# Kernel tuning notes

Measured on AMD Instinct MI355X. Metric: run time of the kernel, lower is better.

## Reference

```python
import jax, jax.numpy as jnp
import numpy as np

B, S, D = 8, 1024, 1024
H, DK = 16, 64  # num_heads, d_k; H*DK == D
NEG_INF = 1e29


def setup_inputs() -> dict:
    key = jax.random.key(0)
    ks = jax.random.split(key, 12)
    sc = 1.0 / np.sqrt(D)
    q = jax.random.normal(ks[0], (B, S, D), jnp.float32)
    k = jax.random.normal(ks[1], (B, S, D), jnp.float32)
    v = jax.random.normal(ks[2], (B, S, D), jnp.float32)
    # causal mask, broadcast per batch (mask==0 positions are masked out)
    mask = jnp.broadcast_to(jnp.tril(jnp.ones((S, S), jnp.int32)), (B, S, S))
    Wq = jax.random.normal(ks[3], (D, D), jnp.float32) * sc
    bq = jax.random.normal(ks[4], (D,), jnp.float32) * 0.01
    Wk = jax.random.normal(ks[5], (D, D), jnp.float32) * sc
    bk = jax.random.normal(ks[6], (D,), jnp.float32) * 0.01
    Wv = jax.random.normal(ks[7], (D, D), jnp.float32) * sc
    bv = jax.random.normal(ks[8], (D,), jnp.float32) * 0.01
    Wo = jax.random.normal(ks[9], (D, D), jnp.float32) * sc
    bo = jax.random.normal(ks[10], (D,), jnp.float32) * 0.01
    return {"q": q, "k": k, "v": v, "mask": mask,
            "Wq": Wq, "bq": bq, "Wk": Wk, "bk": bk,
            "Wv": Wv, "bv": bv, "Wo": Wo, "bo": bo}


def reference(q, k, v, mask, Wq, bq, Wk, bk, Wv, bv, Wo, bo):
    # Linear projections (torch Linear: x @ W.T + b)
    q1 = q @ Wq.T + bq
    k1 = k @ Wk.T + bk
    v1 = v @ Wv.T + bv
    # [B, S, D] -> [B, H, S, DK]
    def split_heads(x):
        return x.reshape(B, S, H, DK).transpose(0, 2, 1, 3)
    q3, k3, v3 = split_heads(q1), split_heads(k1), split_heads(v1)
    # scores [B, H, S, S]
    scores = jnp.einsum('bhqd,bhkd->bhqk', q3, k3) / jnp.sqrt(jnp.float32(DK))
    scores = jnp.where(mask[:, None, :, :] == 0, -NEG_INF, scores)
    probs = jax.nn.softmax(scores, axis=-1)
    attn = jnp.einsum('bhqk,bhkd->bhqd', probs, v3)  # [B, H, S, DK]
    out = attn.transpose(0, 2, 1, 3).reshape(B, S, D)
    return out @ Wo.T + bo
```

## Files before the change

### kernel.cpp

```cpp
#include <hip/hip_runtime.h>
#include <hip/hip_bf16.h>
#include <stdint.h>

constexpr int NB = 8;
constexpr int NS = 1024;
constexpr int ND = 1024;
constexpr int NH = 16;
constexpr int NDK = 64;
constexpr int NKT = ND / 64;

typedef __bf16 bf16_t;
typedef __attribute__((ext_vector_type(8))) __bf16 bf16x8;
typedef __attribute__((ext_vector_type(4))) __bf16 bf16x4;
typedef __attribute__((ext_vector_type(4))) float f32x4;
typedef __attribute__((ext_vector_type(16))) float f32x16;

#define GLL16(g, s) __builtin_amdgcn_global_load_lds( \
    (const __attribute__((address_space(1))) void*)(g), \
    (__attribute__((address_space(3))) void*)(s), 16, 0, 0)

__device__ __forceinline__ unsigned cvtpk_bf16(float lo, float hi) {
  unsigned r;
  asm("v_cvt_pk_bf16_f32 %0, %1, %2" : "=v"(r) : "v"(lo), "v"(hi));
  return r;
}

__device__ __forceinline__ void cvt_body(const float* __restrict__ s,
                                         bf16_t* __restrict__ d, long n) {
  long i0 = (long)(blockIdx.x * blockDim.x + threadIdx.x) * 4;
  long step = (long)gridDim.x * blockDim.x * 4;
  for (long i = i0; i < n; i += step) {
    float4 f = *(const float4*)(s + i);
    bf16x4 o;
    o[0] = (bf16_t)f.x; o[1] = (bf16_t)f.y; o[2] = (bf16_t)f.z; o[3] = (bf16_t)f.w;
    *(bf16x4*)(d + i) = o;
  }
}

__global__ __launch_bounds__(256) void cvt4_kernel(const float* s0, bf16_t* d0,
                                                   const float* s1, bf16_t* d1,
                                                   const float* s2, bf16_t* d2,
                                                   const float* s3, bf16_t* d3, long n) {
  const float* s = blockIdx.y == 0 ? s0 : blockIdx.y == 1 ? s1 : blockIdx.y == 2 ? s2 : s3;
  bf16_t* d = blockIdx.y == 0 ? d0 : blockIdx.y == 1 ? d1 : blockIdx.y == 2 ? d2 : d3;
  cvt_body(s, d, n);
}

__global__ __launch_bounds__(512, 2) void gemm_qkv(
    const float* A0, const bf16_t* W0, const float* b0, bf16_t* C0,
    const float* A1, const bf16_t* W1, const float* b1, bf16_t* C1,
    const float* A2, const bf16_t* W2, const float* b2, bf16_t* C2) {
  __shared__ bf16_t S[2 * 16384 + 3 * 8192];
  const int o = blockIdx.x;
  const int xcd = o & 7, s = o >> 3;
  const int bx = s & 7, u = s >> 3;
  const int zby = xcd + 8 * u;
  const int z = zby >> 5, by = zby & 31;
  const float* A = z == 0 ? A0 : z == 1 ? A1 : A2;
  const bf16_t* W = z == 0 ? W0 : z == 1 ? W1 : W2;
  const float* bb = z == 0 ? b0 : z == 1 ? b1 : b2;
  bf16_t* C = z == 0 ? C0 : z == 1 ? C1 : C2;

  const int tid = threadIdx.x;
  const int l = tid & 63, w = tid >> 6;
  const int wr = w >> 1, wc = w & 1;
  const int g = l >> 4, r = l & 15;
  const int m0 = by * 256, n0 = bx * 128;
  const int wbase = w * 512;

  bf16_t* Ab = S;
  bf16_t* Bb = S + 32768;

  float4 faA[8], faB[8];
  auto issueA = [&](int t, float4 (&dst)[8]) {
#pragma unroll
    for (int it = 0; it < 4; ++it) {
      const float* p = A + (size_t)(m0 + it * 64 + (tid >> 3)) * ND + t * 64 + (tid & 7) * 8;
      dst[it * 2]     = *(const float4*)p;
      dst[it * 2 + 1] = *(const float4*)(p + 4);
    }
  };
  auto writeA = [&](int ab, float4 (&src)[8]) {
#pragma unroll
    for (int it = 0; it < 4; ++it) {
      int row = it * 64 + (tid >> 3), c = tid & 7;
      bf16x8 ov;
      ov[0] = (bf16_t)src[it * 2].x;     ov[1] = (bf16_t)src[it * 2].y;
      ov[2] = (bf16_t)src[it * 2].z;     ov[3] = (bf16_t)src[it * 2].w;
      ov[4] = (bf16_t)src[it * 2 + 1].x; ov[5] = (bf16_t)src[it * 2 + 1].y;
      ov[6] = (bf16_t)src[it * 2 + 1].z; ov[7] = (bf16_t)src[it * 2 + 1].w;
      *(bf16x8*)(Ab + ab * 16384 + row * 64 + ((c ^ (row & 7)) << 3)) = ov;
    }
  };
  auto stageB = [&](int qb, int t) {
#pragma unroll
    for (int it = 0; it < 2; ++it) {
      int idx = it * 512 + tid;
      int row = idx >> 3, c = (idx & 7) ^ (row & 7);
      GLL16(W + (size_t)(n0 + row) * ND + (t << 6) + c * 8,
            Bb + qb * 8192 + it * 4096 + wbase);
    }
  };

  f32x4 acc[4][4] = {};

  issueA(0, faA);
  issueA(1, faB);
  stageB(0, 0);
  stageB(1, 1);
  asm volatile("s_waitcnt vmcnt(2)" ::: "memory");
  __builtin_amdgcn_sched_barrier(0);
  writeA(0, faA);
  asm volatile("s_waitcnt lgkmcnt(0)" ::: "memory");
  __builtin_amdgcn_s_barrier();

  auto bodyT = [&](int t, float4 (&fiss)[8], float4 (&fwr)[8]) {
    if (t + 2 < NKT) issueA(t + 2, fiss);
    __builtin_amdgcn_sched_barrier(0);
    if (t + 2 < NKT) stageB((t + 2) % 3, t + 2);
    __builtin_amdgcn_sched_barrier(0);

    const bf16_t* a_ = Ab + (t & 1) * 16384;
    const bf16_t* b_ = Bb + (t % 3) * 8192;
#pragma unroll
    for (int kk = 0; kk < 2; ++kk) {
      bf16x8 af[4], bw[4];
#pragma unroll
      for (int m = 0; m < 4; ++m) {
        int row = wr * 64 + m * 16 + r;
        af[m] = *(const bf16x8*)(a_ + row * 64 + (((kk * 4 + g) ^ (row & 7)) << 3));
      }
#pragma unroll
      for (int n = 0; n < 4; ++n) {
        int row = wc * 64 + n * 16 + r;
        bw[n] = *(const bf16x8*)(b_ + row * 64 + (((kk * 4 + g) ^ (row & 7)) << 3));
      }
      __builtin_amdgcn_s_setprio(1);
#pragma unroll
      for (int m = 0; m < 4; ++m)
#pragma unroll
        for (int n = 0; n < 4; ++n)
          acc[m][n] = __builtin_amdgcn_mfma_f32_16x16x32_bf16(af[m], bw[n], acc[m][n], 0, 0, 0);
      __builtin_amdgcn_s_setprio(0);
    }

    if (t + 2 < NKT)      asm volatile("s_waitcnt vmcnt(10)" ::: "memory");
    else                  asm volatile("s_waitcnt vmcnt(0)" ::: "memory");
    __builtin_amdgcn_sched_barrier(0);
    if (t + 1 < NKT) writeA((t + 1) & 1, fwr);
    asm volatile("s_waitcnt lgkmcnt(0)" ::: "memory");
    __builtin_amdgcn_s_barrier();
  };

#pragma unroll 1
  for (int tt = 0; tt < NKT; tt += 2) {
    bodyT(tt, faA, faB);
    bodyT(tt + 1, faB, faA);
  }

  if (z == 2) {
#pragma unroll
    for (int n = 0; n < 4; ++n) {
      int col = n0 + wc * 64 + n * 16 + r;
      int hh = col >> 6, dk = col & 63;
      float bv = bb[col];
#pragma unroll
      for (int m = 0; m < 4; ++m) {
        int row0 = m0 + wr * 64 + m * 16 + g * 4;
        int b_ = row0 >> 10, s0 = row0 & 1023;
        bf16x4 o4;
#pragma unroll
        for (int j = 0; j < 4; ++j) o4[j] = (bf16_t)(acc[m][n][j] + bv);
        *(bf16x4*)(C + (((size_t)b_ * 16 + hh) * 64 + dk) * 1024 + s0) = o4;
      }
    }
  } else {
#pragma unroll
    for (int n = 0; n < 4; ++n) {
      int col = n0 + wc * 64 + n * 16 + r;
      float bv = bb[col];
#pragma unroll
      for (int m = 0; m < 4; ++m) {
        int row0 = m0 + wr * 64 + m * 16 + g * 4;
#pragma unroll
        for (int j = 0; j < 4; ++j)
          C[(size_t)(row0 + j) * ND + col] = (bf16_t)(acc[m][n][j] + bv);
      }
    }
  }
}

__global__ __launch_bounds__(512, 2) void gemm_bt(const bf16_t* __restrict__ A,
                                                  const bf16_t* __restrict__ W,
                                                  const float* __restrict__ bias,
                                                  float* __restrict__ Cout,
                                                  int M, int N, int K) {
  __shared__ bf16_t S[3 * 24576];
  const int o = blockIdx.x;
  const int xcd = o & 7, s = o >> 3;
  const int bx = s & 7, u = s >> 3;
  const int by = xcd + 8 * u;

  const int tid = threadIdx.x;
  const int l = tid & 63, w = tid >> 6;
  const int wr = w >> 1, wc = w & 1;
  const int g = l >> 4, r = l & 15;
  const int m0 = by * 256, n0 = bx * 128;
  const int wbase = w * 512;

  auto stageA2 = [&](int q, int t, int half) {
#pragma unroll
    for (int it = half * 2; it < half * 2 + 2; ++it) {
      int idx = it * 512 + tid;
      int row = idx >> 3, c = (idx & 7) ^ (row & 7);
      GLL16(A + (size_t)(m0 + row) * K + (t << 6) + c * 8,
            S + q * 24576 + it * 4096 + wbase);
    }
  };
  auto stageB2 = [&](int q, int t) {
#pragma unroll
    for (int it = 0; it < 2; ++it) {
      int idx = it * 512 + tid;
      int row = idx >> 3, c = (idx & 7) ^ (row & 7);
      GLL16(W + (size_t)(n0 + row) * K + (t << 6) + c * 8,
            S + q * 24576 + 16384 + it * 4096 + wbase);
    }
  };

  f32x4 acc[4][4] = {};
  const int NKT2 = K >> 6;

  stageA2(0, 0, 0); stageA2(0, 0, 1); stageB2(0, 0);
  stageA2(1, 1, 0); stageA2(1, 1, 1); stageB2(1, 1);

  int q = 0;
  for (int t = 0; t < NKT2; ++t) {
    const bool pf = (t + 2 < NKT2);
    int q2 = q + 2; if (q2 >= 3) q2 -= 3;

    if (t + 1 < NKT2) asm volatile("s_waitcnt vmcnt(6)" ::: "memory");
    else              asm volatile("s_waitcnt vmcnt(0)" ::: "memory");
    __builtin_amdgcn_s_barrier();

    const bf16_t* a_ = S + q * 24576;
    const bf16_t* b_ = a_ + 16384;

#pragma unroll
    for (int kk = 0; kk < 2; ++kk) {
      bf16x8 bw[4];
#pragma unroll
      for (int n = 0; n < 4; ++n) {
        int row = wc * 64 + n * 16 + r;
        bw[n] = *(const bf16x8*)(b_ + row * 64 + (((kk * 4 + g) ^ (row & 7)) << 3));
      }
#pragma unroll
      for (int mh = 0; mh < 2; ++mh) {
        bf16x8 af[2];
#pragma unroll
        for (int i = 0; i < 2; ++i) {
          int row = wr * 64 + (mh * 2 + i) * 16 + r;
          af[i] = *(const bf16x8*)(a_ + row * 64 + (((kk * 4 + g) ^ (row & 7)) << 3));
        }
        if (pf) {
          int ph = kk * 2 + mh;
          if (ph == 0)      stageA2(q2, t + 2, 0);
          else if (ph == 1) stageA2(q2, t + 2, 1);
          else if (ph == 2) stageB2(q2, t + 2);
        }
        __builtin_amdgcn_s_barrier();
        asm volatile("s_waitcnt lgkmcnt(0)" ::: "memory");
        __builtin_amdgcn_sched_barrier(0);
        __builtin_amdgcn_s_setprio(1);
#pragma unroll
        for (int i = 0; i < 2; ++i)
#pragma unroll
          for (int n = 0; n < 4; ++n)
            acc[mh * 2 + i][n] = __builtin_amdgcn_mfma_f32_16x16x32_bf16(
                af[i], bw[n], acc[mh * 2 + i][n], 0, 0, 0);
        __builtin_amdgcn_s_setprio(0);
        __builtin_amdgcn_sched_barrier(0);
      }
    }
    ++q; if (q >= 3) q -= 3;
  }

#pragma unroll
  for (int n = 0; n < 4; ++n) {
    int col = n0 + wc * 64 + n * 16 + r;
    float bv = bias[col];
#pragma unroll
    for (int m = 0; m < 4; ++m) {
      int row0 = m0 + wr * 64 + m * 16 + g * 4;
#pragma unroll
      for (int j = 0; j < 4; ++j)
        Cout[(size_t)(row0 + j) * N + col] = acc[m][n][j] + bv;
    }
  }
}

__global__ __launch_bounds__(256, 2) void attn_kernel(const bf16_t* __restrict__ Q1,
                                                      const bf16_t* __restrict__ K1,
                                                      const bf16_t* __restrict__ V1t,
                                                      bf16_t* __restrict__ attn) {
  __shared__ bf16_t Kt[2][64 * 64];
  __shared__ bf16_t Vt[2][64 * 64];

  const int tid = threadIdx.x;
  const int l = tid & 63, w = tid >> 6;
  const int q32 = l & 31, h5 = l >> 5;

  const int o = blockIdx.x;
  const int os = (o & 7) * 64 + (o >> 3);
  const int pair = os & 3, hb = os >> 2;
  const int h = hb & 15, b = hb >> 4;

  constexpr float SC = 0.18033688011112042f;
  const bf16_t* vbase = V1t + ((size_t)(b * 16 + h) * 64) * 1024;

  auto stageKV = [&](int kt2, int pb) {
    const int k0 = kt2 * 64;
#pragma unroll
    for (int it = 0; it < 2; ++it) {
      int idx = it * 256 + tid;
      int row = idx >> 3, c = (idx & 7) ^ (row & 7);
      GLL16(K1 + ((size_t)b * NS + k0 + row) * ND + h * 64 + c * 8,
            &Kt[pb][it * 2048 + w * 512]);
      GLL16(vbase + (size_t)row * 1024 + k0 + c * 8,
            &Vt[pb][it * 2048 + w * 512]);
    }
  };

  for (int ph = 0; ph < 2; ++ph) {
    const int qt = ph ? (7 - pair) : pair;
    const int qrow_g = qt * 128 + w * 32 + q32;

    const bf16_t* qptr = Q1 + ((size_t)b * NS + qrow_g) * ND + h * 64;
    bf16x8 qf[4];
#pragma unroll
    for (int ds = 0; ds < 4; ++ds) {
      qf[ds] = *(const bf16x8*)(qptr + ds * 16 + h5 * 8);
#pragma unroll
      for (int i = 0; i < 8; ++i) qf[ds][i] = (bf16_t)((float)qf[ds][i] * SC);
    }

    float mrun = -1e30f, lrun = 0.f;
    f32x16 oacc0 = {}, oacc1 = {};

    __syncthreads();

    const int nkt = 2 * qt + 2;
    stageKV(0, 0);

    for (int kt = 0; kt < nkt; ++kt) {
      const int p = kt & 1;
      const int k0 = kt * 64;

      __syncthreads();

      if (kt + 1 < nkt) stageKV(kt + 1, p ^ 1);

      f32x16 s0 = {}, s1 = {};
      __builtin_amdgcn_s_setprio(1);
#pragma unroll
      for (int ds = 0; ds < 4; ++ds) {
        int dk2b = (ds * 16 + h5 * 8) * 2;
        {
          int row = q32;
          bf16x8 kf = *(const bf16x8*)((char*)Kt[p] + row * 128 + (dk2b ^ ((row & 7) << 4)));
          s0 = __builtin_amdgcn_mfma_f32_32x32x16_bf16(kf, qf[ds], s0, 0, 0, 0);
        }
        {
          int row = 32 + q32;
          bf16x8 kf = *(const bf16x8*)((char*)Kt[p] + row * 128 + (dk2b ^ ((row & 7) << 4)));
          s1 = __builtin_amdgcn_mfma_f32_32x32x16_bf16(kf, qf[ds], s1, 0, 0, 0);
        }
      }
      __builtin_amdgcn_s_setprio(0);

      if (kt >= 2 * qt) {
#pragma unroll
        for (int reg = 0; reg < 16; ++reg) {
          int key = k0 + (reg & 3) + 8 * (reg >> 2) + 4 * h5;
          if (key > qrow_g) s0[reg] = -1e30f;
          if (key + 32 > qrow_g) s1[reg] = -1e30f;
        }
      }

      float mx = s0[0];
#pragma unroll
      for (int i = 1; i < 16; ++i) mx = fmaxf(mx, s0[i]);
#pragma unroll
      for (int i = 0; i < 16; ++i) mx = fmaxf(mx, s1[i]);
      mx = fmaxf(mx, __shfl_xor(mx, 32));

      if (!__all(mx <= mrun + 8.0f)) {
        float m_new = fmaxf(mrun, mx);
        float esc = __builtin_amdgcn_exp2f(mrun - m_new);
        mrun = m_new;
        lrun *= esc;
#pragma unroll
        for (int i = 0; i < 16; ++i) { oacc0[i] *= esc; oacc1[i] *= esc; }
      }

      float rsum = 0.f;
#pragma unroll
      for (int i = 0; i < 16; ++i) { s0[i] = __builtin_amdgcn_exp2f(s0[i] - mrun); rsum += s0[i]; }
#pragma unroll
      for (int i = 0; i < 16; ++i) { s1[i] = __builtin_amdgcn_exp2f(s1[i] - mrun); rsum += s1[i]; }
      rsum += __shfl_xor(rsum, 32);
      lrun += rsum;

      bf16x8 pf[4];
#pragma unroll
      for (int ks = 0; ks < 4; ++ks) {
        const int base = (ks & 1) * 8;
        unsigned ca, cb, cc, cd;
        if (ks < 2) {
          ca = cvtpk_bf16(s0[base + 0], s0[base + 1]);
          cb = cvtpk_bf16(s0[base + 2], s0[base + 3]);
          cc = cvtpk_bf16(s0[base + 4], s0[base + 5]);
          cd = cvtpk_bf16(s0[base + 6], s0[base + 7]);
        } else {
          ca = cvtpk_bf16(s1[base + 0], s1[base + 1]);
          cb = cvtpk_bf16(s1[base + 2], s1[base + 3]);
          cc = cvtpk_bf16(s1[base + 4], s1[base + 5]);
          cd = cvtpk_bf16(s1[base + 6], s1[base + 7]);
        }
        asm volatile("v_permlane32_swap_b32 %0, %1" : "+v"(ca), "+v"(cc));
        asm volatile("v_permlane32_swap_b32 %0, %1" : "+v"(cb), "+v"(cd));
        union { unsigned u[4]; bf16x8 v; } pw;
        pw.u[0] = ca; pw.u[1] = cb; pw.u[2] = cc; pw.u[3] = cd;
        pf[ks] = pw.v;
      }

      __builtin_amdgcn_s_setprio(1);
#pragma unroll
      for (int ks = 0; ks < 4; ++ks) {
        int key2b = (ks * 16 + h5 * 8) * 2;
        {
          int row = q32;
          bf16x8 vf = *(const bf16x8*)((char*)Vt[p] + row * 128 + (key2b ^ ((row & 7) << 4)));
          oacc0 = __builtin_amdgcn_mfma_f32_32x32x16_bf16(vf, pf[ks], oacc0, 0, 0, 0);
        }
        {
          int row = 32 + q32;
          bf16x8 vf = *(const bf16x8*)((char*)Vt[p] + row * 128 + (key2b ^ ((row & 7) << 4)));
          oacc1 = __builtin_amdgcn_mfma_f32_32x32x16_bf16(vf, pf[ks], oacc1, 0, 0, 0);
        }
      }
      __builtin_amdgcn_s_setprio(0);
    }

    float linv = 1.0f / lrun;
    bf16_t* optr = attn + ((size_t)b * NS + qrow_g) * ND + h * 64;
#pragma unroll
    for (int rr = 0; rr < 4; ++rr) {
      bf16x4 o4a, o4b;
#pragma unroll
      for (int j = 0; j < 4; ++j) {
        o4a[j] = (bf16_t)(oacc0[rr * 4 + j] * linv);
        o4b[j] = (bf16_t)(oacc1[rr * 4 + j] * linv);
      }
      *(bf16x4*)(optr + rr * 8 + h5 * 4) = o4a;
      *(bf16x4*)(optr + 32 + rr * 8 + h5 * 4) = o4b;
    }
  }
}

extern "C" void kernel_launch(void* const* d_in, const int* in_sizes, int n_in,
                              void* d_out, int out_size, void* d_ws, size_t ws_size,
                              hipStream_t stream) {
  const float* q  = (const float*)d_in[0];
  const float* k  = (const float*)d_in[1];
  const float* v  = (const float*)d_in[2];
  const float* Wq = (const float*)d_in[4];
  const float* bq = (const float*)d_in[5];
  const float* Wk = (const float*)d_in[6];
  const float* bk = (const float*)d_in[7];
  const float* Wv = (const float*)d_in[8];
  const float* bv = (const float*)d_in[9];
  const float* Wo = (const float*)d_in[10];
  const float* bo = (const float*)d_in[11];
  float* out = (float*)d_out;

  const size_t NX = (size_t)NB * NS * ND;
  const size_t NW = (size_t)ND * ND;
  char* ws = (char*)d_ws;
  size_t off = 0;
  auto alloc = [&](size_t bytes) {
    char* p = ws + off;
    off += (bytes + 255) & ~(size_t)255;
    return p;
  };
  bf16_t* wqb = (bf16_t*)alloc(NW * 2);
  bf16_t* wkb = (bf16_t*)alloc(NW * 2);
  bf16_t* wvb = (bf16_t*)alloc(NW * 2);
  bf16_t* wob = (bf16_t*)alloc(NW * 2);
  bf16_t* q1  = (bf16_t*)alloc(NX * 2);
  bf16_t* k1  = (bf16_t*)alloc(NX * 2);
  bf16_t* v1t = (bf16_t*)alloc(NX * 2);
  bf16_t* at  = (bf16_t*)alloc(NX * 2);

  dim3 blk(256);
  cvt4_kernel<<<dim3(128, 4), blk, 0, stream>>>(Wq, wqb, Wk, wkb, Wv, wvb, Wo, wob, (long)NW);

  gemm_qkv<<<dim3(768), dim3(512), 0, stream>>>(
      q, wqb, bq, q1, k, wkb, bk, k1, v, wvb, bv, v1t);

  attn_kernel<<<dim3(512), dim3(256), 0, stream>>>(q1, k1, v1t, at);

  gemm_bt<<<dim3(256), dim3(512), 0, stream>>>(at, wob, bo, out, NB * NS, ND, ND);
}
```

Measured before the change: 144.2 us.

## Double the attention key tile to 128 and tree-reduce softmax max/sum

The flash-attention loop now handles 128 keys per iteration instead of 64, staging two 64-key K/V sub-tiles per buffer. This halves the number of barriers, online-softmax rescale checks and loop overheads per query tile. It also interleaves P conversion with the PV MFMAs and uses tree reductions for the max and sum. In exchange it doubles LDS use (64 KB per block) and raises register pressure, which may lower occupancy under the 256x2 launch bound. Because the causal diagonal is now 128 keys wide, more fully masked work is done on the final tile.

```diff
diff --git a/kernel.cpp b/kernel.cpp
--- a/kernel.cpp
+++ b/kernel.cpp
@@ -23,6 +23,24 @@
   unsigned r;
   asm("v_cvt_pk_bf16_f32 %0, %1, %2" : "=v"(r) : "v"(lo), "v"(hi));
   return r;
+}
+
+__device__ __forceinline__ float tmax16(const f32x16& v) {
+  float a0 = fmaxf(v[0], v[1]),  a1 = fmaxf(v[2], v[3]);
+  float a2 = fmaxf(v[4], v[5]),  a3 = fmaxf(v[6], v[7]);
+  float a4 = fmaxf(v[8], v[9]),  a5 = fmaxf(v[10], v[11]);
+  float a6 = fmaxf(v[12], v[13]), a7 = fmaxf(v[14], v[15]);
+  float b0 = fmaxf(a0, a1), b1 = fmaxf(a2, a3);
+  float b2 = fmaxf(a4, a5), b3 = fmaxf(a6, a7);
+  return fmaxf(fmaxf(b0, b1), fmaxf(b2, b3));
+}
+__device__ __forceinline__ float tsum16(const f32x16& v) {
+  float a0 = v[0] + v[1],  a1 = v[2] + v[3];
+  float a2 = v[4] + v[5],  a3 = v[6] + v[7];
+  float a4 = v[8] + v[9],  a5 = v[10] + v[11];
+  float a6 = v[12] + v[13], a7 = v[14] + v[15];
+  float b0 = a0 + a1, b1 = a2 + a3, b2 = a4 + a5, b3 = a6 + a7;
+  return (b0 + b1) + (b2 + b3);
 }
 
 __device__ __forceinline__ void cvt_body(const float* __restrict__ s,
@@ -302,8 +320,8 @@
                                                       const bf16_t* __restrict__ K1,
                                                       const bf16_t* __restrict__ V1t,
                                                       bf16_t* __restrict__ attn) {
-  __shared__ bf16_t Kt[2][64 * 64];
-  __shared__ bf16_t Vt[2][64 * 64];
+  __shared__ bf16_t Kt[2][2][64 * 64];
+  __shared__ bf16_t Vt[2][2][64 * 64];
 
   const int tid = threadIdx.x;
   const int l = tid & 63, w = tid >> 6;
@@ -318,15 +336,18 @@
   const bf16_t* vbase = V1t + ((size_t)(b * 16 + h) * 64) * 1024;
 
   auto stageKV = [&](int kt2, int pb) {
-    const int k0 = kt2 * 64;
-#pragma unroll
-    for (int it = 0; it < 2; ++it) {
-      int idx = it * 256 + tid;
-      int row = idx >> 3, c = (idx & 7) ^ (row & 7);
-      GLL16(K1 + ((size_t)b * NS + k0 + row) * ND + h * 64 + c * 8,
-            &Kt[pb][it * 2048 + w * 512]);
-      GLL16(vbase + (size_t)row * 1024 + k0 + c * 8,
-            &Vt[pb][it * 2048 + w * 512]);
+    const int k0 = kt2 * 128;
+#pragma unroll
+    for (int sub = 0; sub < 2; ++sub) {
+#pragma unroll
+      for (int it = 0; it < 2; ++it) {
+        int idx = it * 256 + tid;
+        int row = idx >> 3, c = (idx & 7) ^ (row & 7);
+        GLL16(K1 + ((size_t)b * NS + k0 + sub * 64 + row) * ND + h * 64 + c * 8,
+              &Kt[pb][sub][it * 2048 + w * 512]);
+        GLL16(vbase + (size_t)row * 1024 + k0 + sub * 64 + c * 8,
+              &Vt[pb][sub][it * 2048 + w * 512]);
+      }
     }
   };
 
@@ -348,49 +369,45 @@
 
     __syncthreads();
 
-    const int nkt = 2 * qt + 2;
+    const int nkt = qt + 1;
     stageKV(0, 0);
 
     for (int kt = 0; kt < nkt; ++kt) {
       const int p = kt & 1;
-      const int k0 = kt * 64;
+      const int k0 = kt * 128;
 
       __syncthreads();
 
       if (kt + 1 < nkt) stageKV(kt + 1, p ^ 1);
 
-      f32x16 s0 = {}, s1 = {};
+      f32x16 sarr[4] = {{}, {}, {}, {}};
       __builtin_amdgcn_s_setprio(1);
 #pragma unroll
-      for (int ds = 0; ds < 4; ++ds) {
-        int dk2b = (ds * 16 + h5 * 8) * 2;
-        {
-          int row = q32;
-          bf16x8 kf = *(const bf16x8*)((char*)Kt[p] + row * 128 + (dk2b ^ ((row & 7) << 4)));
-          s0 = __builtin_amdgcn_mfma_f32_32x32x16_bf16(kf, qf[ds], s0, 0, 0, 0);
+      for (int st = 0; st < 4; ++st) {
+        const int kh = st >> 1;
+        const int row = (st & 1) * 32 + q32;
+#pragma unroll
+        for (int ds = 0; ds < 4; ++ds) {
+          int dk2b = (ds * 16 + h5 * 8) * 2;
+          bf16x8 kf = *(const bf16x8*)((char*)Kt[p][kh] + row * 128 + (dk2b ^ ((row & 7) << 4)));
+          sarr[st] = __builtin_amdgcn_mfma_f32_32x32x16_bf16(kf, qf[ds], sarr[st], 0, 0, 0);
         }
-        {
-          int row = 32 + q32;
-          bf16x8 kf = *(const bf16x8*)((char*)Kt[p] + row * 128 + (dk2b ^ ((row & 7) << 4)));
-          s1 = __builtin_amdgcn_mfma_f32_32x32x16_bf16(kf, qf[ds], s1, 0, 0, 0);
-        }
       }
       __builtin_amdgcn_s_setprio(0);
 
-      if (kt >= 2 * qt) {
-#pragma unroll
-        for (int reg = 0; reg < 16; ++reg) {
-          int key = k0 + (reg & 3) + 8 * (reg >> 2) + 4 * h5;
-          if (key > qrow_g) s0[reg] = -1e30f;
-          if (key + 32 > qrow_g) s1[reg] = -1e30f;
-        }
-      }
-
-      float mx = s0[0];
-#pragma unroll
-      for (int i = 1; i < 16; ++i) mx = fmaxf(mx, s0[i]);
-#pragma unroll
-      for (int i = 0; i < 16; ++i) mx = fmaxf(mx, s1[i]);
+      if (kt == nkt - 1) {
+#pragma unroll
+        for (int st = 0; st < 4; ++st)
+#pragma unroll
+          for (int reg = 0; reg < 16; ++reg) {
+            int key = k0 + st * 32 + (reg & 3) + 8 * (reg >> 2) + 4 * h5;
+            if (key > qrow_g) sarr[st][reg] = -1e30f;
+          }
+      }
+
+      float m0 = tmax16(sarr[0]), m1 = tmax16(sarr[1]);
+      float m2 = tmax16(sarr[2]), m3 = tmax16(sarr[3]);
+      float mx = fmaxf(fmaxf(m0, m1), fmaxf(m2, m3));
       mx = fmaxf(mx, __shfl_xor(mx, 32));
 
       if (!__all(mx <= mrun + 8.0f)) {
@@ -402,50 +419,42 @@
         for (int i = 0; i < 16; ++i) { oacc0[i] *= esc; oacc1[i] *= esc; }
       }
 
-      float rsum = 0.f;
-#pragma unroll
-      for (int i = 0; i < 16; ++i) { s0[i] = __builtin_amdgcn_exp2f(s0[i] - mrun); rsum += s0[i]; }
-#pragma unroll
-      for (int i = 0; i < 16; ++i) { s1[i] = __builtin_amdgcn_exp2f(s1[i] - mrun); rsum += s1[i]; }
+#pragma unroll
+      for (int st = 0; st < 4; ++st)
+#pragma unroll
+        for (int i = 0; i < 16; ++i)
+          sarr[st][i] = __builtin_amdgcn_exp2f(sarr[st][i] - mrun);
+      float r0 = tsum16(sarr[0]) + tsum16(sarr[1]);
+      float r1 = tsum16(sarr[2]) + tsum16(sarr[3]);
+      float rsum = r0 + r1;
       rsum += __shfl_xor(rsum, 32);
       lrun += rsum;
 
-      bf16x8 pf[4];
-#pragma unroll
-      for (int ks = 0; ks < 4; ++ks) {
-        const int base = (ks & 1) * 8;
-        unsigned ca, cb, cc, cd;
-        if (ks < 2) {
-          ca = cvtpk_bf16(s0[base + 0], s0[base + 1]);
-          cb = cvtpk_bf16(s0[base + 2], s0[base + 3]);
-          cc = cvtpk_bf16(s0[base + 4], s0[base + 5]);
-          cd = cvtpk_bf16(s0[base + 6], s0[base + 7]);
-        } else {
-          ca = cvtpk_bf16(s1[base + 0], s1[base + 1]);
-          cb = cvtpk_bf16(s1[base + 2], s1[base + 3]);
-          cc = cvtpk_bf16(s1[base + 4], s1[base + 5]);
-          cd = cvtpk_bf16(s1[base + 6], s1[base + 7]);
-        }
+      __builtin_amdgcn_s_setprio(1);
+#pragma unroll
+      for (int ks2 = 0; ks2 < 8; ++ks2) {
+        const int st = ks2 >> 1;
+        const int base = (ks2 & 1) * 8;
+        unsigned ca = cvtpk_bf16(sarr[st][base + 0], sarr[st][base + 1]);
+        unsigned cb = cvtpk_bf16(sarr[st][base + 2], sarr[st][base + 3]);
+        unsigned cc = cvtpk_bf16(sarr[st][base + 4], sarr[st][base + 5]);
+        unsigned cd = cvtpk_bf16(sarr[st][base + 6], sarr[st][base + 7]);
         asm volatile("v_permlane32_swap_b32 %0, %1" : "+v"(ca), "+v"(cc));
         asm volatile("v_permlane32_swap_b32 %0, %1" : "+v"(cb), "+v"(cd));
         union { unsigned u[4]; bf16x8 v; } pw;
         pw.u[0] = ca; pw.u[1] = cb; pw.u[2] = cc; pw.u[3] = cd;
-        pf[ks] = pw.v;
-      }
-
-      __builtin_amdgcn_s_setprio(1);
-#pragma unroll
-      for (int ks = 0; ks < 4; ++ks) {
-        int key2b = (ks * 16 + h5 * 8) * 2;
+
+        const int kh2 = ks2 >> 2;
+        const int key2b = ((ks2 & 3) * 16 + h5 * 8) * 2;
         {
           int row = q32;
-          bf16x8 vf = *(const bf16x8*)((char*)Vt[p] + row * 128 + (key2b ^ ((row & 7) << 4)));
-          oacc0 = __builtin_amdgcn_mfma_f32_32x32x16_bf16(vf, pf[ks], oacc0, 0, 0, 0);
+          bf16x8 vf = *(const bf16x8*)((char*)Vt[p][kh2] + row * 128 + (key2b ^ ((row & 7) << 4)));
+          oacc0 = __builtin_amdgcn_mfma_f32_32x32x16_bf16(vf, pw.v, oacc0, 0, 0, 0);
         }
         {
           int row = 32 + q32;
-          bf16x8 vf = *(const bf16x8*)((char*)Vt[p] + row * 128 + (key2b ^ ((row & 7) << 4)));
-          oacc1 = __builtin_amdgcn_mfma_f32_32x32x16_bf16(vf, pf[ks], oacc1, 0, 0, 0);
+          bf16x8 vf = *(const bf16x8*)((char*)Vt[p][kh2] + row * 128 + (key2b ^ ((row & 7) << 4)));
+          oacc1 = __builtin_amdgcn_mfma_f32_32x32x16_bf16(vf, pw.v, oacc1, 0, 0, 0);
         }
       }
       __builtin_amdgcn_s_setprio(0);
```

After: 148.6 us. +3.0%, slower.
